# Performance work log

Hardware: AMD Instinct MI355X
Metric: run time of the kernel (lower is better)

## Reference

```python
import jax, jax.numpy as jnp
import numpy as np

V, E, DZ, C = 32000, 8, 30, 10
CH = (4, 8, 8)
K = (3, 3, 3)
S = (2, 2, 1)
B, L = 512, 4096


def setup_inputs() -> dict:
    key = jax.random.key(0)
    ks = jax.random.split(key, 12)
    inp = {
        "input_ids": jax.random.randint(ks[0], (B, L), 0, V),
        "attention_mask": jnp.ones((B, L), dtype=jnp.float32),
        "z": jax.random.normal(ks[1], (DZ,), dtype=jnp.float32),
        "embed_table": jax.random.normal(ks[2], (V, E), dtype=jnp.float32),
        # ensemble-stacked frozen conv weights, torch Conv1d layout [O, I, K]
        "W1": jax.random.normal(ks[3], (DZ, CH[0], E, K[0]), dtype=jnp.float32) * 0.2,
        "b1": jax.random.normal(ks[4], (DZ, CH[0]), dtype=jnp.float32) * 0.1,
        "W2": jax.random.normal(ks[5], (DZ, CH[1], CH[0], K[1]), dtype=jnp.float32) * 0.2,
        "b2": jax.random.normal(ks[6], (DZ, CH[1]), dtype=jnp.float32) * 0.1,
        "W3": jax.random.normal(ks[7], (DZ, CH[2], CH[1], K[2]), dtype=jnp.float32) * 0.2,
        "b3": jax.random.normal(ks[8], (DZ, CH[2]), dtype=jnp.float32) * 0.1,
        "Wh": jax.random.normal(ks[9], (DZ, C, CH[2]), dtype=jnp.float32) * 0.2,
        "bh": jax.random.normal(ks[10], (DZ, C), dtype=jnp.float32) * 0.1,
    }
    return inp


def _conv1d(x, w, stride):
    # x: [B, Cin, L], w: [Cout, Cin, K]
    return jax.lax.conv_general_dilated(
        x, w, window_strides=(stride,), padding="VALID",
        dimension_numbers=("NCH", "OIH", "NCH"))


def _forward(input_ids, attention_mask, z, embed_table,
             W1, b1, W2, b2, W3, b3, Wh, bh):
    x = embed_table[input_ids]                      # [B, L, E]
    x = x * attention_mask[..., None]
    x = jnp.transpose(x, (0, 2, 1))                 # [B, E, L]

    def one_net(w1, c1, w2, c2, w3, c3, wh, ch):
        h = jax.nn.relu(_conv1d(x, w1, S[0]) + c1[None, :, None])
        h = jax.nn.relu(_conv1d(h, w2, S[1]) + c2[None, :, None])
        h = jax.nn.relu(_conv1d(h, w3, S[2]) + c3[None, :, None])
        pooled = h.mean(axis=-1)                    # [B, ch3]
        return pooled @ wh.T + ch                   # [B, C]

    pis = jax.vmap(one_net)(W1, b1, W2, b2, W3, b3, Wh, bh)  # [Dz, B, C]
    return jnp.einsum("dbc,d->bc", pis, z)          # [B, C]


def reference(input_ids, attention_mask, z, embed_table,
              W1, b1, W2, b2, W3, b3, Wh, bh):
    return _forward(input_ids, attention_mask, z, embed_table,
                    W1, b1, W2, b2, W3, b3, Wh, bh)
```

## Files before the change

### kernel.cpp

```cpp
#include <hip/hip_runtime.h>
#include <stdint.h>


typedef _Float16 f16;
typedef f16 f16x2 __attribute__((ext_vector_type(2)));
typedef f16 f16x4 __attribute__((ext_vector_type(4)));
typedef f16 f16x8 __attribute__((ext_vector_type(8)));
typedef float f32x4 __attribute__((ext_vector_type(4)));

#define H1S 2064
#define H2S 1034
#define REG 8272

__global__ __launch_bounds__(256) void prep_kernel(
    const int* __restrict__ ids, const float* __restrict__ mask,
    const float* __restrict__ tbl,
    const float* __restrict__ W1, const float* __restrict__ W2,
    const float* __restrict__ W3,
    f16* __restrict__ x, f16* __restrict__ a1p,
    f16* __restrict__ a2, f16* __restrict__ a3) {
  const int blk = blockIdx.x;
  if (blk < 4096) {
    const int b  = blk >> 3;
    const int l0 = ((blk & 7) * 256 + threadIdx.x) * 2;
    const int2   iv = *(const int2*)(ids + (size_t)b * 4096 + l0);
    const float2 mv = *(const float2*)(mask + (size_t)b * 4096 + l0);
    const float4* t4 = (const float4*)tbl;
    const float4 a0 = t4[(size_t)iv.x * 2], A1 = t4[(size_t)iv.x * 2 + 1];
    const float4 c0 = t4[(size_t)iv.y * 2], C1 = t4[(size_t)iv.y * 2 + 1];
    const float r0[8] = {a0.x, a0.y, a0.z, a0.w, A1.x, A1.y, A1.z, A1.w};
    const float r1[8] = {c0.x, c0.y, c0.z, c0.w, C1.x, C1.y, C1.z, C1.w};
    f16* xb = x + (size_t)b * 8 * 4096 + l0;
    #pragma unroll
    for (int e = 0; e < 8; ++e) {
      f16x2 p; p.x = (f16)(r0[e] * mv.x); p.y = (f16)(r1[e] * mv.y);
      *(f16x2*)(xb + e * 4096) = p;
    }
  } else {
    const int i = (blk - 4096) * 256 + threadIdx.x;
    if (i < 960) {
      const int g = i >> 6, l = i & 63;
      const int kg = l >> 4, col = l & 15;
      f16x8 v;
      #pragma unroll
      for (int j = 0; j < 8; ++j) {
        const int e = 2 * kg + (j >> 2), tap = j & 3;
        float val = 0.0f;
        if (col < 8 && tap < 3) {
          const int d = g * 2 + (col >> 2), c = col & 3;
          val = W1[d * 96 + c * 24 + e * 3 + tap];
        }
        v[j] = (f16)val;
      }
      *(f16x8*)(a1p + ((size_t)g * 64 + l) * 8) = v;
    } else if (i < 2880) {
      const int idx = i - 960, d = idx >> 6, lane = idx & 63;
      const int quad = lane >> 4, m = lane & 15;
      f16x8 v;
      #pragma unroll
      for (int j = 0; j < 8; ++j) {
        float val = 0.0f;
        if (m < 8)  { if (j < 3)           val = W2[d * 96 + m * 12 + quad * 3 + j]; }
        else        { if (j >= 2 && j < 5) val = W2[d * 96 + (m - 8) * 12 + quad * 3 + (j - 2)]; }
        v[j] = (f16)val;
      }
      *(f16x8*)(a2 + ((size_t)d * 64 + lane) * 8) = v;
    } else if (i < 4800) {
      const int idx = i - 2880, d = idx >> 6, lane = idx & 63;
      const int quad = lane >> 4, m = lane & 15;
      f16x8 v;
      #pragma unroll
      for (int j = 0; j < 8; ++j) {
        const int c2 = quad * 2 + (j >> 2), t = j & 3;
        float val = 0.0f;
        if (m < 8)  { if (t < 3)  val = W3[d * 192 + m * 24 + c2 * 3 + t]; }
        else        { if (t >= 1) val = W3[d * 192 + (m - 8) * 24 + c2 * 3 + (t - 1)]; }
        v[j] = (f16)val;
      }
      *(f16x8*)(a3 + ((size_t)d * 64 + lane) * 8) = v;
    }
  }
}

__global__ __launch_bounds__(512, 8) void ensemble_f16_kernel(
    const f16* __restrict__ x,
    const f16* __restrict__ a1p,
    const f16* __restrict__ a2,
    const f16* __restrict__ a3,
    const float* __restrict__ z,
    const float* __restrict__ b1, const float* __restrict__ b2,
    const float* __restrict__ b3,
    const float* __restrict__ Wh, const float* __restrict__ bh,
    float* __restrict__ part)
{
  const int tid = threadIdx.x;
  const int swz  = ((blockIdx.x & 7) * 960) + (blockIdx.x >> 3);
  const int b    = swz / 15;
  const int pair = swz - b * 15;
  const int d0   = 2 * pair;

  __shared__ __align__(16) f16 smemh[2 * REG];
  __shared__ float red[2][32];

  const int w = tid >> 6, lane = tid & 63, quad = lane >> 4, n = lane & 15;
  const int g = w >> 2, wv = w & 3;
  const int d = d0 + g;

  if (tid < 128)
    smemh[(tid >> 6) * REG + ((tid >> 4) & 3) * H1S + 2048 + (tid & 15)] = (f16)0.0f;

  {
    const f16x8 bw1 = *(const f16x8*)(a1p + ((size_t)pair * 64 + lane) * 8);
    float bias = 0.0f;
    if (n < 8) bias = b1[(d0 + (n >> 2)) * 4 + (n & 3)];
    const f32x4 c1i = {bias, bias, bias, bias};
    const char* xc = (const char*)(x + (size_t)b * 32768) + quad * 16384 + 4 * n;
    f16x4* h1w = (f16x4*)smemh + (n >> 2) * (REG / 4) + (n & 3) * (H1S / 4) + quad;
    #pragma unroll 8
    for (int i = 0; i < 16; ++i) {
      const int t = w + 8 * i;
      const uint32_t o = 64u * (uint32_t)t;
      union { f16x8 v; uint32_t dw[4]; } u;
      u.dw[0] = *(const uint32_t*)(xc + o);
      u.dw[1] = *(const uint32_t*)(xc + o + 4);
      u.dw[2] = *(const uint32_t*)(xc + o + 8192);
      u.dw[3] = *(const uint32_t*)(xc + o + 8192 + 4);
      const f32x4 D = __builtin_amdgcn_mfma_f32_16x16x32_f16(u.v, bw1, c1i, 0, 0, 0);
      if (n < 8) {
        f16x4 p;
        p.x = (f16)fmaxf(D[0], 0.0f); p.y = (f16)fmaxf(D[1], 0.0f);
        p.z = (f16)fmaxf(D[2], 0.0f); p.w = (f16)fmaxf(D[3], 0.0f);
        h1w[4 * t] = p;
      }
    }
  }
  __syncthreads();

  f32x4 Ci[8];
  {
    const f16x8 af2 = *(const f16x8*)(a2 + ((size_t)d * 64 + lane) * 8);
    const f32x4 cinit2 = *(const f32x4*)(b2 + d * 8 + (quad & 1) * 4);
    const f16x4* h14 = (const f16x4*)smemh + g * (REG / 4);
    const int qbase = quad * (H1S / 4);
    #pragma unroll
    for (int i = 0; i < 8; ++i) {
      const int t = wv + 4 * i;
      const f16x4 lo = h14[qbase + 16 * t + n];
      const f16x4 hi = h14[qbase + 16 * t + n + 1];
      const f16x8 bv = __builtin_shufflevector(lo, hi, 0, 1, 2, 3, 4, 5, 6, 7);
      Ci[i] = __builtin_amdgcn_mfma_f32_16x16x32_f16(af2, bv, cinit2, 0, 0, 0);
    }
  }
  __syncthreads();

  {
    f16* h2f = smemh + g * REG;
    const int shift = quad >> 1;
    const int c2b   = (quad & 1) * 4;
    #pragma unroll
    for (int i = 0; i < 8; ++i) {
      const int t  = wv + 4 * i;
      const int jl = 32 * t + 2 * n + shift;
      #pragma unroll
      for (int r = 0; r < 4; ++r)
        h2f[(c2b + r) * H2S + jl] = (f16)fmaxf(Ci[i][r], 0.0f);
    }
    if (tid < 160) {
      const int rg = tid / 80, ix = tid - rg * 80;
      smemh[rg * REG + (ix / 10) * H2S + 1024 + (ix % 10)] = (f16)0.0f;
    }
  }
  __syncthreads();

  float pool4[4] = {0.0f, 0.0f, 0.0f, 0.0f};
  {
    const f16x8 af3 = *(const f16x8*)(a3 + ((size_t)d * 64 + lane) * 8);
    const f32x4 cinit3 = *(const f32x4*)(b3 + d * 8 + (quad & 1) * 4);
    const f16* h2f = smemh + g * REG;
    const int c2a = quad * 2;
    #pragma unroll
    for (int i = 0; i < 8; ++i) {
      const int t = wv + 4 * i;
      const f16* bp = h2f + c2a * H2S + 32 * t + 2 * n;
      union { f16x8 v; f16x2 q[4]; } u;
      u.q[0] = *(const f16x2*)bp;
      u.q[1] = *(const f16x2*)(bp + 2);
      u.q[2] = *(const f16x2*)(bp + H2S);
      u.q[3] = *(const f16x2*)(bp + H2S + 2);
      const f32x4 C = __builtin_amdgcn_mfma_f32_16x16x32_f16(af3, u.v, cinit3, 0, 0, 0);
      const int pl = 32 * t + 2 * n + (quad >> 1);
      if (pl < 1021) {
        #pragma unroll
        for (int r = 0; r < 4; ++r) pool4[r] += fmaxf(C[r], 0.0f);
      }
    }
  }

  {
    #pragma unroll
    for (int r = 0; r < 4; ++r) pool4[r] += __shfl_xor(pool4[r], 1, 64);
    #pragma unroll
    for (int r = 0; r < 4; ++r) pool4[r] += __shfl_xor(pool4[r], 2, 64);
    #pragma unroll
    for (int r = 0; r < 4; ++r) pool4[r] += __shfl_xor(pool4[r], 4, 64);
    #pragma unroll
    for (int r = 0; r < 4; ++r) pool4[r] += __shfl_xor(pool4[r], 8, 64);
    #pragma unroll
    for (int r = 0; r < 4; ++r) pool4[r] += __shfl_xor(pool4[r], 32, 64);
    if ((lane & 47) == 0) {
      const int cg = (lane >> 4) & 1;
      #pragma unroll
      for (int r = 0; r < 4; ++r) red[g][wv * 8 + cg * 4 + r] = pool4[r];
    }
  }
  __syncthreads();

  if ((w == 0 || w == 4) && lane < 10) {
    const int gg = w >> 2;
    const int dd = d0 + gg;
    float acc = bh[dd * 10 + lane];
    #pragma unroll
    for (int c3 = 0; c3 < 8; ++c3) {
      const float pooled = red[gg][c3]      + red[gg][8 + c3]
                         + red[gg][16 + c3] + red[gg][24 + c3];
      acc = fmaf(pooled * (1.0f / 1021.0f), Wh[dd * 80 + lane * 8 + c3], acc);
    }
    part[((size_t)dd * 512 + b) * 10 + lane] = z[dd] * acc;
  }
}

__global__ __launch_bounds__(256) void reduce30_kernel(
    const float* __restrict__ part,
    float* __restrict__ out)
{
  const int i = blockIdx.x * 256 + threadIdx.x;
  float s = 0.0f;
  #pragma unroll
  for (int dd = 0; dd < 30; ++dd) s += part[dd * 5120 + i];
  out[i] = s;
}

__global__ __launch_bounds__(256, 6) void ensemble_kernel(
    const int* __restrict__ ids, const float* __restrict__ mask,
    const float* __restrict__ z, const float* __restrict__ tbl,
    const float* __restrict__ W1, const float* __restrict__ b1,
    const float* __restrict__ W2, const float* __restrict__ b2,
    const float* __restrict__ W3, const float* __restrict__ b3,
    const float* __restrict__ Wh, const float* __restrict__ bh,
    float* __restrict__ part)
{
  const int tid  = threadIdx.x;
  const int half = blockIdx.x & 1;
  const int bd   = blockIdx.x >> 1;
  const int b    = bd & 511;
  const int d    = bd >> 9;

  __shared__ float smem[4128];
  __shared__ float red[32];
  __shared__ float pooled[8];

  const int l_lo = half ? 1024 : 0;
  const int l_hi = half ? 2047 : 1029;
  const int j_lo = half ? 512  : 0;
  const int j_hi = half ? 1023 : 514;
  const int o_lo = half ? 512  : 0;
  const int o_hi = half ? 1021 : 512;

  const int*    idrow = ids  + (size_t)b * 4096;
  const float*  mrow  = mask + (size_t)b * 4096;
  const float4* tbl4  = (const float4*)tbl;
  const float*  w1p = W1 + d * 96;
  const float*  w2p = W2 + d * 96;
  const float*  w3p = W3 + d * 192;

  {
    float bia[4];
    #pragma unroll
    for (int c = 0; c < 4; ++c) bia[c] = b1[d * 4 + c];

    #pragma unroll 1
    for (int pass = 0; pass < 2; ++pass) {
      const int l0 = l_lo + 2 * tid + 512 * pass;
      const int p0 = 2 * l0;
      const int4   iv = *(const int4*)(idrow + p0);
      const float4 mv = *(const float4*)(mrow + p0);
      int i4; float m4;
      if (p0 + 4 < 4096) { i4 = idrow[p0 + 4]; m4 = mrow[p0 + 4]; }
      else               { i4 = 0;              m4 = 0.0f; }

      const int   pid[5] = {iv.x, iv.y, iv.z, iv.w, i4};
      const float pm[5]  = {mv.x, mv.y, mv.z, mv.w, m4};

      float a0[4], a1v[4];
      #pragma unroll
      for (int c = 0; c < 4; ++c) { a0[c] = bia[c]; a1v[c] = bia[c]; }

      #pragma unroll
      for (int q = 0; q < 5; ++q) {
        const float4 va = tbl4[(size_t)pid[q] * 2];
        const float4 vb = tbl4[(size_t)pid[q] * 2 + 1];
        const float xe[8] = {va.x * pm[q], va.y * pm[q], va.z * pm[q], va.w * pm[q],
                             vb.x * pm[q], vb.y * pm[q], vb.z * pm[q], vb.w * pm[q]};
        if (q <= 2) {
          #pragma unroll
          for (int c = 0; c < 4; ++c)
            #pragma unroll
            for (int e = 0; e < 8; ++e)
              a0[c] = fmaf(xe[e], w1p[c * 24 + e * 3 + q], a0[c]);
        }
        if (q >= 2) {
          #pragma unroll
          for (int c = 0; c < 4; ++c)
            #pragma unroll
            for (int e = 0; e < 8; ++e)
              a1v[c] = fmaf(xe[e], w1p[c * 24 + e * 3 + (q - 2)], a1v[c]);
        }
      }
      const int rel = l0 - l_lo;
      if (l0 + 1 < l_hi) {
        #pragma unroll
        for (int c = 0; c < 4; ++c)
          *(float2*)(smem + c * 1032 + rel) =
              make_float2(fmaxf(a0[c], 0.0f), fmaxf(a1v[c], 0.0f));
      } else if (l0 < l_hi) {
        #pragma unroll
        for (int c = 0; c < 4; ++c)
          smem[c * 1032 + rel] = fmaxf(a0[c], 0.0f);
      }
    }
    const int lt = l_lo + 1024 + tid;
    if (lt < l_hi) {
      float a0[4];
      #pragma unroll
      for (int c = 0; c < 4; ++c) a0[c] = bia[c];
      #pragma unroll
      for (int k = 0; k < 3; ++k) {
        const int p = 2 * lt + k;
        const int id = idrow[p];
        const float m = mrow[p];
        const float4 va = tbl4[(size_t)id * 2];
        const float4 vb = tbl4[(size_t)id * 2 + 1];
        const float xe[8] = {va.x*m, va.y*m, va.z*m, va.w*m,
                             vb.x*m, vb.y*m, vb.z*m, vb.w*m};
        #pragma unroll
        for (int cc = 0; cc < 4; ++cc)
          #pragma unroll
          for (int e = 0; e < 8; ++e)
            a0[cc] = fmaf(xe[e], w1p[cc * 24 + e * 3 + k], a0[cc]);
      }
      #pragma unroll
      for (int c = 0; c < 4; ++c)
        smem[c * 1032 + 1024 + tid] = fmaxf(a0[c], 0.0f);
    }
  }
  __syncthreads();

  float acc2[8][2], acc2t[8];
  {
    #pragma unroll
    for (int c2 = 0; c2 < 8; ++c2) {
      const float bb = b2[d * 8 + c2];
      acc2[c2][0] = bb; acc2[c2][1] = bb; acc2t[c2] = bb;
    }
    const int rel2  = 4 * tid;
    const bool tail2 = tid < (j_hi - j_lo - 512);
    #pragma unroll 1
    for (int c1 = 0; c1 < 4; ++c1) {
      float sw[8][3];
      #pragma unroll
      for (int c2 = 0; c2 < 8; ++c2)
        #pragma unroll
        for (int kk = 0; kk < 3; ++kk)
          sw[c2][kk] = w2p[c2 * 12 + c1 * 3 + kk];
      const float* hp = smem + c1 * 1032;
      const float4 h01 = *(const float4*)(hp + rel2);
      const float  h4v = hp[rel2 + 4];
      #pragma unroll
      for (int c2 = 0; c2 < 8; ++c2) {
        acc2[c2][0] = fmaf(h01.x, sw[c2][0], fmaf(h01.y, sw[c2][1],
                      fmaf(h01.z, sw[c2][2], acc2[c2][0])));
        acc2[c2][1] = fmaf(h01.z, sw[c2][0], fmaf(h01.w, sw[c2][1],
                      fmaf(h4v,   sw[c2][2], acc2[c2][1])));
      }
      if (tail2) {
        const float t0 = hp[1024 + 2 * tid], t1 = hp[1025 + 2 * tid],
                    t2 = hp[1026 + 2 * tid];
        #pragma unroll
        for (int c2 = 0; c2 < 8; ++c2)
          acc2t[c2] = fmaf(t0, sw[c2][0], fmaf(t1, sw[c2][1],
                      fmaf(t2, sw[c2][2], acc2t[c2])));
      }
    }
    #pragma unroll
    for (int c2 = 0; c2 < 8; ++c2) {
      acc2[c2][0] = fmaxf(acc2[c2][0], 0.0f);
      acc2[c2][1] = fmaxf(acc2[c2][1], 0.0f);
      acc2t[c2]   = fmaxf(acc2t[c2],   0.0f);
    }
    __syncthreads();
    const int j0 = j_lo + 2 * tid;
    const int jr = 2 * tid;
    if (j0 + 1 < j_hi) {
      #pragma unroll
      for (int c2 = 0; c2 < 8; ++c2)
        *(float2*)(smem + c2 * 516 + jr) = make_float2(acc2[c2][0], acc2[c2][1]);
    } else if (j0 < j_hi) {
      #pragma unroll
      for (int c2 = 0; c2 < 8; ++c2)
        smem[c2 * 516 + jr] = acc2[c2][0];
    }
    if (tid < (j_hi - j_lo - 512)) {
      #pragma unroll
      for (int c2 = 0; c2 < 8; ++c2)
        smem[c2 * 516 + 512 + tid] = acc2t[c2];
    }
  }
  __syncthreads();

  float acc3[8][2];
  #pragma unroll
  for (int cc = 0; cc < 8; ++cc) {
    const float bb = b3[d * 8 + cc];
    acc3[cc][0] = bb; acc3[cc][1] = bb;
  }
  {
    const int rel3 = 2 * tid;
    #pragma unroll 1
    for (int c2 = 0; c2 < 8; ++c2) {
      float sw[8][3];
      #pragma unroll
      for (int cc = 0; cc < 8; ++cc)
        #pragma unroll
        for (int kk = 0; kk < 3; ++kk)
          sw[cc][kk] = w3p[cc * 24 + c2 * 3 + kk];
      const float* hp = smem + c2 * 516;
      const float2 ha = *(const float2*)(hp + rel3);
      const float2 hb = *(const float2*)(hp + rel3 + 2);
      #pragma unroll
      for (int cc = 0; cc < 8; ++cc) {
        acc3[cc][0] = fmaf(ha.x, sw[cc][0], fmaf(ha.y, sw[cc][1],
                      fmaf(hb.x, sw[cc][2], acc3[cc][0])));
        acc3[cc][1] = fmaf(ha.y, sw[cc][0], fmaf(hb.x, sw[cc][1],
                      fmaf(hb.y, sw[cc][2], acc3[cc][1])));
      }
    }
  }
  const int i0 = o_lo + 2 * tid;
  float psum[8];
  #pragma unroll
  for (int cc = 0; cc < 8; ++cc) {
    float s = 0.0f;
    if (i0 < o_hi)     s += fmaxf(acc3[cc][0], 0.0f);
    if (i0 + 1 < o_hi) s += fmaxf(acc3[cc][1], 0.0f);
    psum[cc] = s;
  }

  const int lane = tid & 63;
  const int wid  = tid >> 6;
  #pragma unroll
  for (int c = 0; c < 8; ++c) {
    float v = psum[c];
    #pragma unroll
    for (int off = 32; off > 0; off >>= 1) v += __shfl_down(v, off, 64);
    if (lane == 0) red[wid * 8 + c] = v;
  }
  __syncthreads();
  if (tid < 8)
    pooled[tid] = red[tid] + red[8 + tid] + red[16 + tid] + red[24 + tid];
  __syncthreads();

  if (tid < 10) {
    float acc = (half == 0) ? bh[d * 10 + tid] : 0.0f;
    #pragma unroll
    for (int c3 = 0; c3 < 8; ++c3)
      acc = fmaf(pooled[c3] * (1.0f / 1021.0f), Wh[d * 80 + tid * 8 + c3], acc);
    part[(((size_t)d * 2 + half) * 512 + b) * 10 + tid] = z[d] * acc;
  }
}

__global__ __launch_bounds__(256) void reduce60_kernel(
    const float* __restrict__ part,
    float* __restrict__ out)
{
  const int i = blockIdx.x * 256 + threadIdx.x;
  float s = 0.0f;
  #pragma unroll
  for (int dd = 0; dd < 60; ++dd) s += part[dd * 5120 + i];
  out[i] = s;
}

extern "C" void kernel_launch(void* const* d_in, const int* in_sizes, int n_in,
                              void* d_out, int out_size, void* d_ws, size_t ws_size,
                              hipStream_t stream) {
  const int*   ids  = (const int*)d_in[0];
  const float* mask = (const float*)d_in[1];
  const float* z    = (const float*)d_in[2];
  const float* tbl  = (const float*)d_in[3];
  const float* W1   = (const float*)d_in[4];
  const float* b1   = (const float*)d_in[5];
  const float* W2   = (const float*)d_in[6];
  const float* b2   = (const float*)d_in[7];
  const float* W3   = (const float*)d_in[8];
  const float* b3   = (const float*)d_in[9];
  const float* Wh   = (const float*)d_in[10];
  const float* bh   = (const float*)d_in[11];
  float* out  = (float*)d_out;
  float* part = (float*)d_ws;

  const size_t part_bytes = 1228800;
  const size_t x_bytes    = (size_t)512 * 8 * 4096 * 2;
  const size_t a1_bytes   = 15360;
  const size_t a_bytes    = 30720;
  const size_t need = part_bytes + x_bytes + a1_bytes + 2 * a_bytes;

  if (ws_size >= need) {
    f16* xh  = (f16*)((char*)d_ws + part_bytes);
    f16* a1p = (f16*)((char*)d_ws + part_bytes + x_bytes);
    f16* a2  = (f16*)((char*)d_ws + part_bytes + x_bytes + a1_bytes);
    f16* a3  = (f16*)((char*)d_ws + part_bytes + x_bytes + a1_bytes + a_bytes);
    hipLaunchKernelGGL(prep_kernel, dim3(4096 + 19), dim3(256), 0, stream,
                       ids, mask, tbl, W1, W2, W3, xh, a1p, a2, a3);
    hipLaunchKernelGGL(ensemble_f16_kernel, dim3(512 * 15), dim3(512), 0, stream,
                       xh, a1p, a2, a3, z, b1, b2, b3, Wh, bh, part);
    hipLaunchKernelGGL(reduce30_kernel, dim3(20), dim3(256), 0, stream, part, out);
  } else {
    hipLaunchKernelGGL(ensemble_kernel, dim3(512 * 30 * 2), dim3(256), 0, stream,
                       ids, mask, z, tbl, W1, b1, W2, b2, W3, b3, Wh, bh, part);
    hipLaunchKernelGGL(reduce60_kernel, dim3(20), dim3(256), 0, stream, part, out);
  }
}
```

Baseline: 201.0 us.

## Process four ensemble members per block with rotated shared-memory layout

After: 187.2 us. -6.8%, faster.

```diff
diff --git a/kernel.cpp b/kernel.cpp
--- a/kernel.cpp
+++ b/kernel.cpp
@@ -8,16 +8,12 @@
 typedef f16 f16x8 __attribute__((ext_vector_type(8)));
 typedef float f32x4 __attribute__((ext_vector_type(4)));
 
-#define H1S 2064
-#define H2S 1034
-#define REG 8272
-
 __global__ __launch_bounds__(256) void prep_kernel(
     const int* __restrict__ ids, const float* __restrict__ mask,
     const float* __restrict__ tbl,
     const float* __restrict__ W1, const float* __restrict__ W2,
     const float* __restrict__ W3,
-    f16* __restrict__ x, f16* __restrict__ a1p,
+    f16* __restrict__ x, f16* __restrict__ a1q,
     f16* __restrict__ a2, f16* __restrict__ a3) {
   const int blk = blockIdx.x;
   if (blk < 4096) {
@@ -38,23 +34,22 @@
     }
   } else {
     const int i = (blk - 4096) * 256 + threadIdx.x;
-    if (i < 960) {
+    if (i < 512) {
       const int g = i >> 6, l = i & 63;
       const int kg = l >> 4, col = l & 15;
+      const int d = 4 * g + (col >> 2);
       f16x8 v;
       #pragma unroll
       for (int j = 0; j < 8; ++j) {
         const int e = 2 * kg + (j >> 2), tap = j & 3;
         float val = 0.0f;
-        if (col < 8 && tap < 3) {
-          const int d = g * 2 + (col >> 2), c = col & 3;
-          val = W1[d * 96 + c * 24 + e * 3 + tap];
-        }
+        if (tap < 3 && d < 30)
+          val = W1[d * 96 + (col & 3) * 24 + e * 3 + tap];
         v[j] = (f16)val;
       }
-      *(f16x8*)(a1p + ((size_t)g * 64 + l) * 8) = v;
-    } else if (i < 2880) {
-      const int idx = i - 960, d = idx >> 6, lane = idx & 63;
+      *(f16x8*)(a1q + ((size_t)g * 64 + l) * 8) = v;
+    } else if (i < 2432) {
+      const int idx = i - 512, d = idx >> 6, lane = idx & 63;
       const int quad = lane >> 4, m = lane & 15;
       f16x8 v;
       #pragma unroll
@@ -65,8 +60,8 @@
         v[j] = (f16)val;
       }
       *(f16x8*)(a2 + ((size_t)d * 64 + lane) * 8) = v;
-    } else if (i < 4800) {
-      const int idx = i - 2880, d = idx >> 6, lane = idx & 63;
+    } else if (i < 4352) {
+      const int idx = i - 2432, d = idx >> 6, lane = idx & 63;
       const int quad = lane >> 4, m = lane & 15;
       f16x8 v;
       #pragma unroll
@@ -82,9 +77,9 @@
   }
 }
 
-__global__ __launch_bounds__(512, 8) void ensemble_f16_kernel(
+__global__ __launch_bounds__(1024, 8) void ensemble_f16_kernel(
     const f16* __restrict__ x,
-    const f16* __restrict__ a1p,
+    const f16* __restrict__ a1q,
     const f16* __restrict__ a2,
     const f16* __restrict__ a3,
     const float* __restrict__ z,
@@ -94,31 +89,31 @@
     float* __restrict__ part)
 {
   const int tid = threadIdx.x;
-  const int swz  = ((blockIdx.x & 7) * 960) + (blockIdx.x >> 3);
-  const int b    = swz / 15;
-  const int pair = swz - b * 15;
-  const int d0   = 2 * pair;
-
-  __shared__ __align__(16) f16 smemh[2 * REG];
-  __shared__ float red[2][32];
+  const int swz = ((blockIdx.x & 7) * 512) + (blockIdx.x >> 3);
+  const int b   = swz >> 3;
+  const int G   = swz & 7;
+  const int d_base = 4 * G;
+
+  __shared__ __align__(16) f16 smemh[32768];
+  float* red = (float*)smemh;
 
   const int w = tid >> 6, lane = tid & 63, quad = lane >> 4, n = lane & 15;
-  const int g = w >> 2, wv = w & 3;
-  const int d = d0 + g;
-
-  if (tid < 128)
-    smemh[(tid >> 6) * REG + ((tid >> 4) & 3) * H1S + 2048 + (tid & 15)] = (f16)0.0f;
-
-  {
-    const f16x8 bw1 = *(const f16x8*)(a1p + ((size_t)pair * 64 + lane) * 8);
-    float bias = 0.0f;
-    if (n < 8) bias = b1[(d0 + (n >> 2)) * 4 + (n & 3)];
+  const int gg = w >> 2, wv = w & 3;
+  const int d  = d_base + gg;
+  const int dc = d < 30 ? d : 29;
+
+  {
+    const f16x8 bw1 = *(const f16x8*)(a1q + ((size_t)G * 64 + lane) * 8);
+    const int dn  = d_base + (n >> 2);
+    const int dnc = dn < 30 ? dn : 29;
+    const float bias = b1[dnc * 4 + (n & 3)];
     const f32x4 c1i = {bias, bias, bias, bias};
-    const char* xc = (const char*)(x + (size_t)b * 32768) + quad * 16384 + 4 * n;
-    f16x4* h1w = (f16x4*)smemh + (n >> 2) * (REG / 4) + (n & 3) * (H1S / 4) + quad;
-    #pragma unroll 8
-    for (int i = 0; i < 16; ++i) {
-      const int t = w + 8 * i;
+    const char* xc = (const char*)x + (size_t)b * 65536 + quad * 16384 + 4 * n;
+    f16x4* h1c = (f16x4*)smemh + (n >> 2) * 2048 + (n & 3) * 512;
+    const int rot1 = 5 * (n & 3);
+    #pragma unroll
+    for (int i = 0; i < 8; ++i) {
+      const int t = w + 16 * i;
       const uint32_t o = 64u * (uint32_t)t;
       union { f16x8 v; uint32_t dw[4]; } u;
       u.dw[0] = *(const uint32_t*)(xc + o);
@@ -126,27 +121,27 @@
       u.dw[2] = *(const uint32_t*)(xc + o + 8192);
       u.dw[3] = *(const uint32_t*)(xc + o + 8192 + 4);
       const f32x4 D = __builtin_amdgcn_mfma_f32_16x16x32_f16(u.v, bw1, c1i, 0, 0, 0);
-      if (n < 8) {
-        f16x4 p;
-        p.x = (f16)fmaxf(D[0], 0.0f); p.y = (f16)fmaxf(D[1], 0.0f);
-        p.z = (f16)fmaxf(D[2], 0.0f); p.w = (f16)fmaxf(D[3], 0.0f);
-        h1w[4 * t] = p;
-      }
+      f16x4 p;
+      p.x = (f16)fmaxf(D[0], 0.0f); p.y = (f16)fmaxf(D[1], 0.0f);
+      p.z = (f16)fmaxf(D[2], 0.0f); p.w = (f16)fmaxf(D[3], 0.0f);
+      const int slot = (4 * t + quad + rot1) & 511;
+      h1c[slot] = p;
     }
   }
   __syncthreads();
 
   f32x4 Ci[8];
   {
-    const f16x8 af2 = *(const f16x8*)(a2 + ((size_t)d * 64 + lane) * 8);
-    const f32x4 cinit2 = *(const f32x4*)(b2 + d * 8 + (quad & 1) * 4);
-    const f16x4* h14 = (const f16x4*)smemh + g * (REG / 4);
-    const int qbase = quad * (H1S / 4);
+    const f16x8 af2 = *(const f16x8*)(a2 + ((size_t)dc * 64 + lane) * 8);
+    const f32x4 cinit2 = *(const f32x4*)(b2 + dc * 8 + (quad & 1) * 4);
+    const f16x4* h1r = (const f16x4*)smemh + gg * 2048 + quad * 512;
+    const int rot2 = 5 * quad;
     #pragma unroll
     for (int i = 0; i < 8; ++i) {
       const int t = wv + 4 * i;
-      const f16x4 lo = h14[qbase + 16 * t + n];
-      const f16x4 hi = h14[qbase + 16 * t + n + 1];
+      const int base = 16 * t + n;
+      const f16x4 lo = h1r[(base + rot2) & 511];
+      const f16x4 hi = h1r[(base + 1 + rot2) & 511];
       const f16x8 bv = __builtin_shufflevector(lo, hi, 0, 1, 2, 3, 4, 5, 6, 7);
       Ci[i] = __builtin_amdgcn_mfma_f32_16x16x32_f16(af2, bv, cinit2, 0, 0, 0);
     }
@@ -154,39 +149,39 @@
   __syncthreads();
 
   {
-    f16* h2f = smemh + g * REG;
+    f16* h2b = smemh + gg * 8192;
     const int shift = quad >> 1;
     const int c2b   = (quad & 1) * 4;
     #pragma unroll
     for (int i = 0; i < 8; ++i) {
       const int t  = wv + 4 * i;
-      const int jl = 32 * t + 2 * n + shift;
-      #pragma unroll
-      for (int r = 0; r < 4; ++r)
-        h2f[(c2b + r) * H2S + jl] = (f16)fmaxf(Ci[i][r], 0.0f);
-    }
-    if (tid < 160) {
-      const int rg = tid / 80, ix = tid - rg * 80;
-      smemh[rg * REG + (ix / 10) * H2S + 1024 + (ix % 10)] = (f16)0.0f;
+      const int dw = 16 * t + n;
+      #pragma unroll
+      for (int r = 0; r < 4; ++r) {
+        const int row  = c2b + r;
+        const int slot = (dw + 5 * row) & 511;
+        h2b[row * 1024 + slot * 2 + shift] = (f16)fmaxf(Ci[i][r], 0.0f);
+      }
     }
   }
   __syncthreads();
 
   float pool4[4] = {0.0f, 0.0f, 0.0f, 0.0f};
   {
-    const f16x8 af3 = *(const f16x8*)(a3 + ((size_t)d * 64 + lane) * 8);
-    const f32x4 cinit3 = *(const f32x4*)(b3 + d * 8 + (quad & 1) * 4);
-    const f16* h2f = smemh + g * REG;
+    const f16x8 af3 = *(const f16x8*)(a3 + ((size_t)dc * 64 + lane) * 8);
+    const f32x4 cinit3 = *(const f32x4*)(b3 + dc * 8 + (quad & 1) * 4);
+    const f16* h2r = smemh + gg * 8192;
     const int c2a = quad * 2;
+    const int rotA = 5 * c2a, rotB = 5 * (c2a + 1);
     #pragma unroll
     for (int i = 0; i < 8; ++i) {
-      const int t = wv + 4 * i;
-      const f16* bp = h2f + c2a * H2S + 32 * t + 2 * n;
+      const int t  = wv + 4 * i;
+      const int dw = 16 * t + n;
       union { f16x8 v; f16x2 q[4]; } u;
-      u.q[0] = *(const f16x2*)bp;
-      u.q[1] = *(const f16x2*)(bp + 2);
-      u.q[2] = *(const f16x2*)(bp + H2S);
-      u.q[3] = *(const f16x2*)(bp + H2S + 2);
+      u.q[0] = *(const f16x2*)(h2r + c2a * 1024       + 2 * ((dw     + rotA) & 511));
+      u.q[1] = *(const f16x2*)(h2r + c2a * 1024       + 2 * ((dw + 1 + rotA) & 511));
+      u.q[2] = *(const f16x2*)(h2r + (c2a + 1) * 1024 + 2 * ((dw     + rotB) & 511));
+      u.q[3] = *(const f16x2*)(h2r + (c2a + 1) * 1024 + 2 * ((dw + 1 + rotB) & 511));
       const f32x4 C = __builtin_amdgcn_mfma_f32_16x16x32_f16(af3, u.v, cinit3, 0, 0, 0);
       const int pl = 32 * t + 2 * n + (quad >> 1);
       if (pl < 1021) {
@@ -195,6 +190,7 @@
       }
     }
   }
+  __syncthreads();
 
   {
     #pragma unroll
@@ -210,22 +206,21 @@
     if ((lane & 47) == 0) {
       const int cg = (lane >> 4) & 1;
       #pragma unroll
-      for (int r = 0; r < 4; ++r) red[g][wv * 8 + cg * 4 + r] = pool4[r];
-    }
-  }
-  __syncthreads();
-
-  if ((w == 0 || w == 4) && lane < 10) {
-    const int gg = w >> 2;
-    const int dd = d0 + gg;
-    float acc = bh[dd * 10 + lane];
+      for (int r = 0; r < 4; ++r)
+        red[gg * 32 + wv * 8 + cg * 4 + r] = pool4[r];
+    }
+  }
+  __syncthreads();
+
+  if ((w & 3) == 0 && lane < 10 && d < 30) {
+    float acc = bh[d * 10 + lane];
     #pragma unroll
     for (int c3 = 0; c3 < 8; ++c3) {
-      const float pooled = red[gg][c3]      + red[gg][8 + c3]
-                         + red[gg][16 + c3] + red[gg][24 + c3];
-      acc = fmaf(pooled * (1.0f / 1021.0f), Wh[dd * 80 + lane * 8 + c3], acc);
-    }
-    part[((size_t)dd * 512 + b) * 10 + lane] = z[dd] * acc;
+      const float pooled = red[gg * 32 + c3]      + red[gg * 32 + 8 + c3]
+                         + red[gg * 32 + 16 + c3] + red[gg * 32 + 24 + c3];
+      acc = fmaf(pooled * (1.0f / 1021.0f), Wh[d * 80 + lane * 8 + c3], acc);
+    }
+    part[((size_t)d * 512 + b) * 10 + lane] = z[d] * acc;
   }
 }
 
@@ -509,19 +504,19 @@
 
   const size_t part_bytes = 1228800;
   const size_t x_bytes    = (size_t)512 * 8 * 4096 * 2;
-  const size_t a1_bytes   = 15360;
+  const size_t a1_bytes   = 8192;
   const size_t a_bytes    = 30720;
   const size_t need = part_bytes + x_bytes + a1_bytes + 2 * a_bytes;
 
   if (ws_size >= need) {
     f16* xh  = (f16*)((char*)d_ws + part_bytes);
-    f16* a1p = (f16*)((char*)d_ws + part_bytes + x_bytes);
+    f16* a1q = (f16*)((char*)d_ws + part_bytes + x_bytes);
     f16* a2  = (f16*)((char*)d_ws + part_bytes + x_bytes + a1_bytes);
     f16* a3  = (f16*)((char*)d_ws + part_bytes + x_bytes + a1_bytes + a_bytes);
-    hipLaunchKernelGGL(prep_kernel, dim3(4096 + 19), dim3(256), 0, stream,
-                       ids, mask, tbl, W1, W2, W3, xh, a1p, a2, a3);
-    hipLaunchKernelGGL(ensemble_f16_kernel, dim3(512 * 15), dim3(512), 0, stream,
-                       xh, a1p, a2, a3, z, b1, b2, b3, Wh, bh, part);
+    hipLaunchKernelGGL(prep_kernel, dim3(4096 + 17), dim3(256), 0, stream,
+                       ids, mask, tbl, W1, W2, W3, xh, a1q, a2, a3);
+    hipLaunchKernelGGL(ensemble_f16_kernel, dim3(512 * 8), dim3(1024), 0, stream,
+                       xh, a1q, a2, a3, z, b1, b2, b3, Wh, bh, part);
     hipLaunchKernelGGL(reduce30_kernel, dim3(20), dim3(256), 0, stream, part, out);
   } else {
     hipLaunchKernelGGL(ensemble_kernel, dim3(512 * 30 * 2), dim3(256), 0, stream,
```
